# Performance work log

Hardware: AMD Instinct MI355X
Metric: run time of the kernel (lower is better)

## Reference

```python
import jax, jax.numpy as jnp
import numpy as np

N, IN_FEATS, OUT_FEATS = 8192, 512, 256


def setup_inputs() -> dict:
    key = jax.random.key(0)
    k1, k2, k3, k4 = jax.random.split(key, 4)
    feature_mat = jax.random.normal(k1, (N, IN_FEATS), dtype=jnp.float32)
    # Xavier-uniform style init for W and W2
    limW = float(np.sqrt(6.0 / (IN_FEATS + OUT_FEATS)))
    W = jax.random.uniform(k2, (IN_FEATS, OUT_FEATS), minval=-limW, maxval=limW, dtype=jnp.float32)
    limW2 = float(np.sqrt(6.0 / (2 * OUT_FEATS + 1)))
    W2 = jax.random.uniform(k3, (2 * OUT_FEATS, 1), minval=-limW2, maxval=limW2, dtype=jnp.float32)
    adj_mat = jax.random.randint(k4, (N, N), 0, 2, dtype=jnp.int32)
    return {"feature_mat": feature_mat, "W": W, "W2": W2, "adj_mat": adj_mat}


def reference(feature_mat, W, W2, adj_mat):
    out_feats = W.shape[1]
    Wh = feature_mat @ W                      # [N, F']
    Wh1 = Wh @ W2[:out_feats, :]              # [N, 1]
    Wh2 = Wh @ W2[out_feats:, :]              # [N, 1]
    e = Wh1 + Wh2.T                           # [N, N] broadcast add
    e = jnp.where(e > 0, e, 0.2 * e)          # leaky_relu(0.2)
    # NOTE: original masks with ZERO (not -inf) before softmax — faithful.
    e = jnp.where(adj_mat > 0, e, jnp.zeros((), dtype=e.dtype))
    attention = jax.nn.softmax(e, axis=1)     # row softmax over all N
    h_prime = attention @ Wh                  # [N, F']
    return jax.nn.relu(h_prime)
```

## Files before the change

### kernel.cpp

```cpp
#include <hip/hip_runtime.h>
#include <cstdint>
#include <cstddef>

#define NR 8192
#define FOUT 256
#define KIN 512
#define KSPLIT 4
#define JCHUNK (NR / KSPLIT)
#define BKJ 64
#define NSTEP (JCHUNK / BKJ)
#define IROWS 64

typedef __attribute__((ext_vector_type(8))) short bf16x8;
typedef __attribute__((ext_vector_type(4))) float f32x4;

__device__ __forceinline__ unsigned f2bf(float x) {
  unsigned u = __float_as_uint(x);
  u += 0x7fffu + ((u >> 16) & 1u);
  return u >> 16;
}
__device__ __forceinline__ float bf2f(unsigned h) {
  return __uint_as_float(h << 16);
}
__device__ __forceinline__ unsigned fkey(float x) {
  unsigned u = __float_as_uint(x);
  return (u & 0x80000000u) ? ~u : (u | 0x80000000u);
}
__device__ __forceinline__ float fkey_dec(unsigned k) {
  return __uint_as_float((k & 0x80000000u) ? (k ^ 0x80000000u) : ~k);
}

#define GLDS(g, l)                                                            \
  __builtin_amdgcn_global_load_lds(                                           \
      (const __attribute__((address_space(1))) unsigned int*)(g),             \
      (__attribute__((address_space(3))) unsigned int*)(l), 16, 0, 0)

__global__ __launch_bounds__(256) void k0_prep(const float* __restrict__ W,
                                               const float* __restrict__ W2,
                                               float* __restrict__ w1,
                                               float* __restrict__ w2,
                                               char* __restrict__ WTbf,
                                               unsigned* __restrict__ maxkey) {
  if (blockIdx.x == 0 && threadIdx.x == 0) *maxkey = 0u;
  int wv = threadIdx.x >> 6, lane = threadIdx.x & 63;
  int k = blockIdx.x * 4 + wv;
  int f4 = lane * 4;
  float4 wr = *(const float4*)(W + (size_t)k * FOUT + f4);
  float4 a = *(const float4*)(W2 + f4);
  float4 b = *(const float4*)(W2 + FOUT + f4);
  float d1 = wr.x * a.x + wr.y * a.y + wr.z * a.z + wr.w * a.w;
  float d2 = wr.x * b.x + wr.y * b.y + wr.z * b.z + wr.w * b.w;
#pragma unroll
  for (int off = 32; off; off >>= 1) {
    d1 += __shfl_xor(d1, off);
    d2 += __shfl_xor(d2, off);
  }
  if (lane == 0) {
    w1[k] = d1;
    w2[k] = d2;
  }
  int kt = k >> 5, kl = k & 31;
  float wv4[4] = {wr.x, wr.y, wr.z, wr.w};
#pragma unroll
  for (int ff = 0; ff < 4; ++ff) {
    int f = f4 + ff;
    size_t addr = (size_t)kt * 16384 + (f >> 4) * 1024 +
                  (((f & 15) | (((kl >> 3) & 3) << 4)) * 16) + (kl & 7) * 2;
    *(unsigned short*)(WTbf + addr) = (unsigned short)f2bf(wv4[ff]);
  }
}

__global__ __launch_bounds__(256) void k2_fused(
    const float* __restrict__ X, const char* __restrict__ WTbf,
    const float* __restrict__ w1, const float* __restrict__ w2,
    char* __restrict__ WhTf, float* __restrict__ Wh1, float* __restrict__ Wh2,
    unsigned* __restrict__ maxkey) {
  __shared__ char smem[2 * 18432 + 4096];
  char* buf0 = smem;
  char* buf1 = smem + 18432;
  char* wlds = smem + 2 * 18432;
  int t = threadIdx.x, wv = t >> 6, lane = t & 63;
  int jb = blockIdx.x * 32;
  int jr = t >> 3, koff = (t & 7) * 4;
  int cA = (jr & 15) | (((koff >> 3) & 3) << 4);
  int swA = cA ^ (((cA >> 4) & 3) << 2);
  int aoff = (jr >> 4) * 1024 + swA * 16 + ((koff & 4) << 1);
  int slotR = lane ^ (((lane >> 4) & 3) << 2);
  const float* xrow = X + (size_t)(jb + jr) * KIN + koff;

  {
    float2 a_ = *(const float2*)(w1 + t * 2);
    float2 b_ = *(const float2*)(w2 + t * 2);
    *(float2*)(wlds + t * 8) = a_;
    *(float2*)(wlds + 2048 + t * 8) = b_;
  }
  __syncthreads();

  float4 st0, st1, st2, st3;
  float d1 = 0.f, d2 = 0.f;
  f32x4 acc[2][4];
#pragma unroll
  for (int a = 0; a < 2; ++a)
#pragma unroll
    for (int b = 0; b < 4; ++b) acc[a][b] = (f32x4){0.f, 0.f, 0.f, 0.f};

#define K2_GLB(KT, BUFW)                                                      \
  do {                                                                        \
    const char* gs_ = WTbf + ((size_t)(KT) << 14) + (wv << 12) + lane * 16;   \
    char* ld_ = (BUFW) + 2048 + (wv << 12);                                   \
    GLDS(gs_, ld_);                                                           \
    GLDS(gs_ + 1024, ld_ + 1024);                                             \
    GLDS(gs_ + 2048, ld_ + 2048);                                             \
    GLDS(gs_ + 3072, ld_ + 3072);                                             \
  } while (0)

#define K2_LDX(KT, ST) (ST) = *(const float4*)(xrow + (KT) * 32)

#define K2_AGEN(ST, BUFW, SNUM)                                               \
  do {                                                                        \
    uint2 a_;                                                                 \
    a_.x = f2bf((ST).x) | (f2bf((ST).y) << 16);                               \
    a_.y = f2bf((ST).z) | (f2bf((ST).w) << 16);                               \
    *(uint2*)((BUFW) + aoff) = a_;                                            \
    float4 wa_ = *(const float4*)(wlds + ((SNUM)*32 + koff) * 4);             \
    float4 wb_ = *(const float4*)(wlds + 2048 + ((SNUM)*32 + koff) * 4);      \
    d1 += (ST).x * wa_.x + (ST).y * wa_.y + (ST).z * wa_.z + (ST).w * wa_.w;  \
    d2 += (ST).x * wb_.x + (ST).y * wb_.y + (ST).z * wb_.z + (ST).w * wb_.w;  \
  } while (0)

#define K2_ITER(S, BUFR, BUFW, STC, STF)                                      \
  do {                                                                        \
    int s_ = (S);                                                             \
    if (s_ + 1 < 16) K2_GLB(s_ + 1, BUFW);                                    \
    K2_LDX((s_ + 3 < 16) ? s_ + 3 : 15, STF);                                 \
    if (s_ + 1 < 16) K2_AGEN(STC, BUFW, s_ + 1);                              \
    bf16x8 a0 = *(const bf16x8*)((BUFR) + slotR * 16);                        \
    bf16x8 a1 = *(const bf16x8*)((BUFR) + 1024 + slotR * 16);                 \
    bf16x8 b0 = *(const bf16x8*)((BUFR) + 2048 + (wv * 4 + 0) * 1024 + lane * 16); \
    bf16x8 b1 = *(const bf16x8*)((BUFR) + 2048 + (wv * 4 + 1) * 1024 + lane * 16); \
    bf16x8 b2 = *(const bf16x8*)((BUFR) + 2048 + (wv * 4 + 2) * 1024 + lane * 16); \
    bf16x8 b3 = *(const bf16x8*)((BUFR) + 2048 + (wv * 4 + 3) * 1024 + lane * 16); \
    acc[0][0] = __builtin_amdgcn_mfma_f32_16x16x32_bf16(a0, b0, acc[0][0], 0, 0, 0); \
    acc[0][1] = __builtin_amdgcn_mfma_f32_16x16x32_bf16(a0, b1, acc[0][1], 0, 0, 0); \
    acc[0][2] = __builtin_amdgcn_mfma_f32_16x16x32_bf16(a0, b2, acc[0][2], 0, 0, 0); \
    acc[0][3] = __builtin_amdgcn_mfma_f32_16x16x32_bf16(a0, b3, acc[0][3], 0, 0, 0); \
    acc[1][0] = __builtin_amdgcn_mfma_f32_16x16x32_bf16(a1, b0, acc[1][0], 0, 0, 0); \
    acc[1][1] = __builtin_amdgcn_mfma_f32_16x16x32_bf16(a1, b1, acc[1][1], 0, 0, 0); \
    acc[1][2] = __builtin_amdgcn_mfma_f32_16x16x32_bf16(a1, b2, acc[1][2], 0, 0, 0); \
    acc[1][3] = __builtin_amdgcn_mfma_f32_16x16x32_bf16(a1, b3, acc[1][3], 0, 0, 0); \
    __builtin_amdgcn_sched_barrier(0);                                        \
    asm volatile("s_waitcnt vmcnt(1)");                                       \
    asm volatile("s_waitcnt lgkmcnt(0)");                                     \
    __builtin_amdgcn_s_barrier();                                             \
    __builtin_amdgcn_sched_barrier(0);                                        \
  } while (0)

  K2_GLB(0, buf0);
  K2_LDX(0, st0);
  K2_LDX(1, st1);
  K2_LDX(2, st2);
  K2_AGEN(st0, buf0, 0);
  __builtin_amdgcn_sched_barrier(0);
  asm volatile("s_waitcnt vmcnt(2)");
  asm volatile("s_waitcnt lgkmcnt(0)");
  __builtin_amdgcn_s_barrier();
  __builtin_amdgcn_sched_barrier(0);

  for (int s4 = 0; s4 < 16; s4 += 4) {
    K2_ITER(s4 + 0, buf0, buf1, st1, st3);
    K2_ITER(s4 + 1, buf1, buf0, st2, st0);
    K2_ITER(s4 + 2, buf0, buf1, st3, st1);
    K2_ITER(s4 + 3, buf1, buf0, st0, st2);
  }
#undef K2_ITER
#undef K2_AGEN
#undef K2_LDX
#undef K2_GLB

  int q = lane >> 4;
#pragma unroll
  for (int mi = 0; mi < 2; ++mi)
#pragma unroll
    for (int nn = 0; nn < 4; ++nn) {
      int u2 = wv * 4 + nn;
      int cell = (lane & 15) | ((((mi * 2) + (q >> 1)) & 3) << 4);
      uint2 v;
      v.x = f2bf(acc[mi][nn].x) | (f2bf(acc[mi][nn].y) << 16);
      v.y = f2bf(acc[mi][nn].z) | (f2bf(acc[mi][nn].w) << 16);
      *(uint2*)(buf0 + 2048 + u2 * 1024 + cell * 16 + ((q & 1) << 3)) = v;
    }
  __syncthreads();
  char* wb = WhTf + (size_t)blockIdx.x * 16384;
#pragma unroll
  for (int q2 = 0; q2 < 4; ++q2) {
    uint4 v = *(const uint4*)(buf0 + 2048 + q2 * 4096 + t * 16);
    *(uint4*)(wb + q2 * 4096 + t * 16) = v;
  }

  d1 += __shfl_xor(d1, 1);
  d1 += __shfl_xor(d1, 2);
  d1 += __shfl_xor(d1, 4);
  d2 += __shfl_xor(d2, 1);
  d2 += __shfl_xor(d2, 2);
  d2 += __shfl_xor(d2, 4);
  if ((t & 7) == 0) {
    Wh1[jb + jr] = d1;
    Wh2[jb + jr] = d2;
  }
  float mx = d2;
#pragma unroll
  for (int off = 32; off >= 8; off >>= 1) mx = fmaxf(mx, __shfl_xor(mx, off));
  __shared__ float red[4];
  if (lane == 0) red[wv] = mx;
  __syncthreads();
  if (t == 0) {
    float bm = fmaxf(fmaxf(red[0], red[1]), fmaxf(red[2], red[3]));
    atomicMax(maxkey, fkey(bm));
  }
}

__device__ __forceinline__ uint2 hv4(int4 aq, float4 wq, float wh1, float m,
                                     float enm, float& z) {
  float s0 = wh1 + wq.x, s1 = wh1 + wq.y, s2 = wh1 + wq.z, s3 = wh1 + wq.w;
  s0 = fmaxf(s0, 0.2f * s0);
  s1 = fmaxf(s1, 0.2f * s1);
  s2 = fmaxf(s2, 0.2f * s2);
  s3 = fmaxf(s3, 0.2f * s3);
  float w0 = aq.x > 0 ? __expf(s0 - m) : enm;
  float w1 = aq.y > 0 ? __expf(s1 - m) : enm;
  float w2 = aq.z > 0 ? __expf(s2 - m) : enm;
  float w3 = aq.w > 0 ? __expf(s3 - m) : enm;
  unsigned h0 = f2bf(w0), h1 = f2bf(w1), h2 = f2bf(w2), h3 = f2bf(w3);
  z += bf2f(h0) + bf2f(h1) + bf2f(h2) + bf2f(h3);
  uint2 r;
  r.x = h0 | (h1 << 16);
  r.y = h2 | (h3 << 16);
  return r;
}
__device__ __forceinline__ uint4 hv8(int4 a0, int4 a1, float4 w0, float4 w1,
                                     float wh1, float m, float enm, float& z) {
  uint2 r0 = hv4(a0, w0, wh1, m, enm, z);
  uint2 r1 = hv4(a1, w1, wh1, m, enm, z);
  return (uint4){r0.x, r0.y, r1.x, r1.y};
}

__global__ __launch_bounds__(512, 4) void k3_attn(
    const int* __restrict__ adj, const char* __restrict__ WhTf,
    const float* __restrict__ Wh1, const float* __restrict__ Wh2,
    const unsigned* __restrict__ maxptr, float* __restrict__ PVp,
    float* __restrict__ Zp) {
  __shared__ char smem[24576];
  char* abuf0 = smem;
  char* abuf1 = smem + 8192;
  char* wlds = smem + 16384;
  int t = threadIdx.x, wv = t >> 6, lane = t & 63;
  int kc = blockIdx.x & 3;
  int ib = blockIdx.x >> 2;
  int ibase = ib * IROWS;
  int jbch = kc * JCHUNK;
  int r0 = t >> 3;
  int j8 = (t & 7) * 8;
  int iglob = ibase + r0;
  float maxwh2 = fkey_dec(*maxptr);
  float wh1 = Wh1[iglob];
  float m = fmaxf(0.f, wh1 + maxwh2);
  float enm = __expf(-m);
  int unitA = (r0 >> 4) * 2 + (j8 >> 5);
  int cA = (r0 & 15) | (((j8 & 31) >> 3) << 4);
  int swA = cA ^ (((cA >> 4) & 3) << 2);
  int aoff = unitA * 1024 + swA * 16;
  int slotR = lane ^ (((lane >> 4) & 3) << 2);
  const int* adjrow = adj + ((size_t)iglob << 13) + jbch + j8;
  const char* bbase = WhTf + ((size_t)(kc * 64) << 14) + (size_t)(wv * 2) * 1024 +
                      (size_t)lane * 16;
  const char* wl = wlds + j8 * 4;

  *(float4*)(wlds + t * 16) = *(const float4*)(Wh2 + jbch + t * 4);
  __syncthreads();

  int4 st0_a, st0_b, st1_a, st1_b;
  f32x4 acc[4][2];
#pragma unroll
  for (int a = 0; a < 4; ++a)
#pragma unroll
    for (int b = 0; b < 2; ++b) acc[a][b] = (f32x4){0.f, 0.f, 0.f, 0.f};
  float zacc = 0.f;

#define K3_LDA(S, ST)                                                         \
  do {                                                                        \
    int sc_ = (S) < NSTEP ? (S) : NSTEP - 1;                                  \
    ST##_a = *(const int4*)(adjrow + sc_ * BKJ);                              \
    ST##_b = *(const int4*)(adjrow + sc_ * BKJ + 4);                          \
  } while (0)

#define K3_ITER(S, AR, AW, STC, DO_HV)                                        \
  do {                                                                        \
    int s_ = (S);                                                             \
    const char* bp_ = bbase + (size_t)(2 * s_) * 16384;                       \
    bf16x8 b00 = *(const bf16x8*)(bp_);                                       \
    bf16x8 b10 = *(const bf16x8*)(bp_ + 1024);                                \
    bf16x8 b01 = *(const bf16x8*)(bp_ + 16384);                               \
    bf16x8 b11 = *(const bf16x8*)(bp_ + 16384 + 1024);                        \
    if (DO_HV) {                                                              \
      float4 wq0_ = *(const float4*)(wl + (s_ + 1) * 256);                    \
      float4 wq1_ = *(const float4*)(wl + (s_ + 1) * 256 + 16);               \
      uint4 a_ = hv8(STC##_a, STC##_b, wq0_, wq1_, wh1, m, enm, zacc);        \
      *(uint4*)((AW) + aoff) = a_;                                            \
    }                                                                         \
    K3_LDA(s_ + 3, STC);                                                      \
    _Pragma("unroll")                                                         \
    for (int rf_ = 0; rf_ < 4; ++rf_) {                                       \
      bf16x8 ak0_ = *(const bf16x8*)((AR) + (rf_ * 2 + 0) * 1024 + slotR * 16); \
      bf16x8 ak1_ = *(const bf16x8*)((AR) + (rf_ * 2 + 1) * 1024 + slotR * 16); \
      acc[rf_][0] = __builtin_amdgcn_mfma_f32_16x16x32_bf16(ak0_, b00, acc[rf_][0], 0, 0, 0); \
      acc[rf_][1] = __builtin_amdgcn_mfma_f32_16x16x32_bf16(ak0_, b10, acc[rf_][1], 0, 0, 0); \
      acc[rf_][0] = __builtin_amdgcn_mfma_f32_16x16x32_bf16(ak1_, b01, acc[rf_][0], 0, 0, 0); \
      acc[rf_][1] = __builtin_amdgcn_mfma_f32_16x16x32_bf16(ak1_, b11, acc[rf_][1], 0, 0, 0); \
    }                                                                         \
    __builtin_amdgcn_sched_barrier(0);                                        \
    asm volatile("s_waitcnt lgkmcnt(0)" ::: "memory");                        \
    __builtin_amdgcn_s_barrier();                                             \
    __builtin_amdgcn_sched_barrier(0);                                        \
  } while (0)

  int4 adj0a = *(const int4*)(adjrow);
  int4 adj0b = *(const int4*)(adjrow + 4);
  K3_LDA(1, st1);
  K3_LDA(2, st0);
  {
    float4 wq0 = *(const float4*)(wl);
    float4 wq1 = *(const float4*)(wl + 16);
    uint4 a0 = hv8(adj0a, adj0b, wq0, wq1, wh1, m, enm, zacc);
    *(uint4*)(abuf0 + aoff) = a0;
  }
  __builtin_amdgcn_sched_barrier(0);
  asm volatile("s_waitcnt lgkmcnt(0)" ::: "memory");
  __builtin_amdgcn_s_barrier();
  __builtin_amdgcn_sched_barrier(0);

  for (int s2 = 0; s2 < NSTEP - 2; s2 += 2) {
    K3_ITER(s2 + 0, abuf0, abuf1, st1, 1);
    K3_ITER(s2 + 1, abuf1, abuf0, st0, 1);
  }
  K3_ITER(NSTEP - 2, abuf0, abuf1, st1, 1);
  K3_ITER(NSTEP - 1, abuf1, abuf0, st0, 0);
#undef K3_ITER
#undef K3_LDA

  zacc += __shfl_xor(zacc, 1);
  zacc += __shfl_xor(zacc, 2);
  zacc += __shfl_xor(zacc, 4);
  if ((t & 7) == 0) Zp[(size_t)kc * NR + iglob] = zacc;
#pragma unroll
  for (int rf = 0; rf < 4; ++rf)
#pragma unroll
    for (int un = 0; un < 2; ++un) {
      int f = (wv * 2 + un) * 16 + (lane & 15);
      int row0 = ibase + rf * 16 + ((lane >> 4) << 2);
      size_t base = ((size_t)kc * NR + row0) * FOUT + f;
      PVp[base + 0 * FOUT] = acc[rf][un].x;
      PVp[base + 1 * FOUT] = acc[rf][un].y;
      PVp[base + 2 * FOUT] = acc[rf][un].z;
      PVp[base + 3 * FOUT] = acc[rf][un].w;
    }
}

__global__ __launch_bounds__(256) void k4_reduce(const float* __restrict__ PVp,
                                                 const float* __restrict__ Zp,
                                                 float* __restrict__ out) {
  int tid = blockIdx.x * 256 + threadIdx.x;
  int i = tid >> 6;
  int f4 = (tid & 63) * 4;
  float z = Zp[i] + Zp[NR + i] + Zp[2 * NR + i] + Zp[3 * NR + i];
  float4 a = {0.f, 0.f, 0.f, 0.f};
#pragma unroll
  for (int c = 0; c < KSPLIT; ++c) {
    float4 p = *(const float4*)(PVp + ((size_t)c * NR + i) * FOUT + f4);
    a.x += p.x;
    a.y += p.y;
    a.z += p.z;
    a.w += p.w;
  }
  float inv = 1.f / z;
  float4 r;
  r.x = fmaxf(a.x * inv, 0.f);
  r.y = fmaxf(a.y * inv, 0.f);
  r.z = fmaxf(a.z * inv, 0.f);
  r.w = fmaxf(a.w * inv, 0.f);
  *(float4*)(out + (size_t)i * FOUT + f4) = r;
}

extern "C" void kernel_launch(void* const* d_in, const int* in_sizes, int n_in,
                              void* d_out, int out_size, void* d_ws,
                              size_t ws_size, hipStream_t stream) {
  const float* X = (const float*)d_in[0];
  const float* W = (const float*)d_in[1];
  const float* W2 = (const float*)d_in[2];
  const int* adj = (const int*)d_in[3];
  float* out = (float*)d_out;
  char* ws = (char*)d_ws;

  const size_t WHT_OFF = 0;
  const size_t WTBF_OFF = (size_t)4 * 1024 * 1024;
  const size_t W1_OFF = WTBF_OFF + 256 * 1024;
  const size_t W2V_OFF = W1_OFF + 2048;
  const size_t WH1_OFF = W2V_OFF + 2048;
  const size_t WH2_OFF = WH1_OFF + 32768;
  const size_t MXK_OFF = WH2_OFF + 32768;
  const size_t ZP_OFF = MXK_OFF + 256;
  const size_t PV_OFF = ZP_OFF + (size_t)KSPLIT * NR * 4;

  char* WhTf = ws + WHT_OFF;
  char* WTbf = ws + WTBF_OFF;
  float* w1 = (float*)(ws + W1_OFF);
  float* w2 = (float*)(ws + W2V_OFF);
  float* Wh1 = (float*)(ws + WH1_OFF);
  float* Wh2 = (float*)(ws + WH2_OFF);
  unsigned* maxkey = (unsigned*)(ws + MXK_OFF);
  float* Zp = (float*)(ws + ZP_OFF);
  float* PVp = (float*)(ws + PV_OFF);

  k0_prep<<<128, 256, 0, stream>>>(W, W2, w1, w2, WTbf, maxkey);
  k2_fused<<<256, 256, 0, stream>>>(X, WTbf, w1, w2, WhTf, Wh1, Wh2, maxkey);
  k3_attn<<<512, 512, 0, stream>>>(adj, WhTf, Wh1, Wh2, maxkey, PVp, Zp);
  k4_reduce<<<2048, 256, 0, stream>>>(PVp, Zp, out);
}
```

Before: 117.9 us.

## Double row tile per attention block and prefetch Wh B-operand one step ahead

The attention kernel now handles 128 rows per block with 1024 threads. Pairs of waves share the same feature columns and split the rows, so each global Wh fragment load feeds twice as many rows. The B-operand loads are also double-buffered in registers and issued one step ahead of the MFMAs to hide global latency. In exchange the grid is halved to 256 blocks, so fewer blocks are resident per CU. The larger block also raises LDS use and register pressure under the 1024-thread launch bound.

```diff
diff --git a/kernel.cpp b/kernel.cpp
--- a/kernel.cpp
+++ b/kernel.cpp
@@ -9,7 +9,7 @@
 #define JCHUNK (NR / KSPLIT)
 #define BKJ 64
 #define NSTEP (JCHUNK / BKJ)
-#define IROWS 64
+#define IROWS 128
 
 typedef __attribute__((ext_vector_type(8))) short bf16x8;
 typedef __attribute__((ext_vector_type(4))) float f32x4;
@@ -244,15 +244,15 @@
   return (uint4){r0.x, r0.y, r1.x, r1.y};
 }
 
-__global__ __launch_bounds__(512, 4) void k3_attn(
+__global__ __launch_bounds__(1024, 4) void k3_attn(
     const int* __restrict__ adj, const char* __restrict__ WhTf,
     const float* __restrict__ Wh1, const float* __restrict__ Wh2,
     const unsigned* __restrict__ maxptr, float* __restrict__ PVp,
     float* __restrict__ Zp) {
-  __shared__ char smem[24576];
+  __shared__ char smem[40960];
   char* abuf0 = smem;
-  char* abuf1 = smem + 8192;
-  char* wlds = smem + 16384;
+  char* abuf1 = smem + 16384;
+  char* wlds = smem + 32768;
   int t = threadIdx.x, wv = t >> 6, lane = t & 63;
   int kc = blockIdx.x & 3;
   int ib = blockIdx.x >> 2;
@@ -271,13 +271,15 @@
   int aoff = unitA * 1024 + swA * 16;
   int slotR = lane ^ (((lane >> 4) & 3) << 2);
   const int* adjrow = adj + ((size_t)iglob << 13) + jbch + j8;
-  const char* bbase = WhTf + ((size_t)(kc * 64) << 14) + (size_t)(wv * 2) * 1024 +
+  int g = wv >> 1, h = wv & 1;
+  const char* bbase = WhTf + ((size_t)(kc * 64) << 14) + (size_t)(2 * g) * 1024 +
                       (size_t)lane * 16;
   const char* wl = wlds + j8 * 4;
 
-  *(float4*)(wlds + t * 16) = *(const float4*)(Wh2 + jbch + t * 4);
+  *(float2*)(wlds + t * 8) = *(const float2*)(Wh2 + jbch + t * 2);
   __syncthreads();
 
+  bf16x8 bA00, bA01, bA10, bA11, bB00, bB01, bB10, bB11;
   int4 st0_a, st0_b, st1_a, st1_b;
   f32x4 acc[4][2];
 #pragma unroll
@@ -285,6 +287,16 @@
 #pragma unroll
     for (int b = 0; b < 2; ++b) acc[a][b] = (f32x4){0.f, 0.f, 0.f, 0.f};
   float zacc = 0.f;
+
+#define K3_LDB(S, B00, B01, B10, B11)                                         \
+  do {                                                                        \
+    int sc_ = (S) < NSTEP ? (S) : NSTEP - 1;                                  \
+    const char* bp_ = bbase + (size_t)(2 * sc_) * 16384;                      \
+    B00 = *(const bf16x8*)(bp_);                                 \
+    B01 = *(const bf16x8*)(bp_ + 16384);                         \
+    B10 = *(const bf16x8*)(bp_ + 1024);                          \
+    B11 = *(const bf16x8*)(bp_ + 16384 + 1024);                  \
+  } while (0)
 
 #define K3_LDA(S, ST)                                                         \
   do {                                                                        \
@@ -293,14 +305,11 @@
     ST##_b = *(const int4*)(adjrow + sc_ * BKJ + 4);                          \
   } while (0)
 
-#define K3_ITER(S, AR, AW, STC, DO_HV)                                        \
+#define K3_ITER(S, AR, AW, BC00, BC01, BC10, BC11, BF00, BF01, BF10, BF11,    \
+                STC, DO_HV)                                                   \
   do {                                                                        \
     int s_ = (S);                                                             \
-    const char* bp_ = bbase + (size_t)(2 * s_) * 16384;                       \
-    bf16x8 b00 = *(const bf16x8*)(bp_);                                       \
-    bf16x8 b10 = *(const bf16x8*)(bp_ + 1024);                                \
-    bf16x8 b01 = *(const bf16x8*)(bp_ + 16384);                               \
-    bf16x8 b11 = *(const bf16x8*)(bp_ + 16384 + 1024);                        \
+    K3_LDB(s_ + 1, BF00, BF01, BF10, BF11);                                   \
     if (DO_HV) {                                                              \
       float4 wq0_ = *(const float4*)(wl + (s_ + 1) * 256);                    \
       float4 wq1_ = *(const float4*)(wl + (s_ + 1) * 256 + 16);               \
@@ -310,12 +319,13 @@
     K3_LDA(s_ + 3, STC);                                                      \
     _Pragma("unroll")                                                         \
     for (int rf_ = 0; rf_ < 4; ++rf_) {                                       \
-      bf16x8 ak0_ = *(const bf16x8*)((AR) + (rf_ * 2 + 0) * 1024 + slotR * 16); \
-      bf16x8 ak1_ = *(const bf16x8*)((AR) + (rf_ * 2 + 1) * 1024 + slotR * 16); \
-      acc[rf_][0] = __builtin_amdgcn_mfma_f32_16x16x32_bf16(ak0_, b00, acc[rf_][0], 0, 0, 0); \
-      acc[rf_][1] = __builtin_amdgcn_mfma_f32_16x16x32_bf16(ak0_, b10, acc[rf_][1], 0, 0, 0); \
-      acc[rf_][0] = __builtin_amdgcn_mfma_f32_16x16x32_bf16(ak1_, b01, acc[rf_][0], 0, 0, 0); \
-      acc[rf_][1] = __builtin_amdgcn_mfma_f32_16x16x32_bf16(ak1_, b11, acc[rf_][1], 0, 0, 0); \
+      int ub_ = (h * 4 + rf_) * 2;                                            \
+      bf16x8 a0_ = *(const bf16x8*)((AR) + (ub_ + 0) * 1024 + slotR * 16);    \
+      bf16x8 a1_ = *(const bf16x8*)((AR) + (ub_ + 1) * 1024 + slotR * 16);    \
+      acc[rf_][0] = __builtin_amdgcn_mfma_f32_16x16x32_bf16(a0_, BC00, acc[rf_][0], 0, 0, 0); \
+      acc[rf_][1] = __builtin_amdgcn_mfma_f32_16x16x32_bf16(a0_, BC10, acc[rf_][1], 0, 0, 0); \
+      acc[rf_][0] = __builtin_amdgcn_mfma_f32_16x16x32_bf16(a1_, BC01, acc[rf_][0], 0, 0, 0); \
+      acc[rf_][1] = __builtin_amdgcn_mfma_f32_16x16x32_bf16(a1_, BC11, acc[rf_][1], 0, 0, 0); \
     }                                                                         \
     __builtin_amdgcn_sched_barrier(0);                                        \
     asm volatile("s_waitcnt lgkmcnt(0)" ::: "memory");                        \
@@ -323,6 +333,7 @@
     __builtin_amdgcn_sched_barrier(0);                                        \
   } while (0)
 
+  K3_LDB(0, bA00, bA01, bA10, bA11);
   int4 adj0a = *(const int4*)(adjrow);
   int4 adj0b = *(const int4*)(adjrow + 4);
   K3_LDA(1, st1);
@@ -339,13 +350,18 @@
   __builtin_amdgcn_sched_barrier(0);
 
   for (int s2 = 0; s2 < NSTEP - 2; s2 += 2) {
-    K3_ITER(s2 + 0, abuf0, abuf1, st1, 1);
-    K3_ITER(s2 + 1, abuf1, abuf0, st0, 1);
-  }
-  K3_ITER(NSTEP - 2, abuf0, abuf1, st1, 1);
-  K3_ITER(NSTEP - 1, abuf1, abuf0, st0, 0);
+    K3_ITER(s2 + 0, abuf0, abuf1, bA00, bA01, bA10, bA11, bB00, bB01, bB10,
+            bB11, st1, 1);
+    K3_ITER(s2 + 1, abuf1, abuf0, bB00, bB01, bB10, bB11, bA00, bA01, bA10,
+            bA11, st0, 1);
+  }
+  K3_ITER(NSTEP - 2, abuf0, abuf1, bA00, bA01, bA10, bA11, bB00, bB01, bB10,
+          bB11, st1, 1);
+  K3_ITER(NSTEP - 1, abuf1, abuf0, bB00, bB01, bB10, bB11, bA00, bA01, bA10,
+          bA11, st0, 0);
 #undef K3_ITER
 #undef K3_LDA
+#undef K3_LDB
 
   zacc += __shfl_xor(zacc, 1);
   zacc += __shfl_xor(zacc, 2);
@@ -355,8 +371,8 @@
   for (int rf = 0; rf < 4; ++rf)
 #pragma unroll
     for (int un = 0; un < 2; ++un) {
-      int f = (wv * 2 + un) * 16 + (lane & 15);
-      int row0 = ibase + rf * 16 + ((lane >> 4) << 2);
+      int f = (2 * g + un) * 16 + (lane & 15);
+      int row0 = ibase + (h * 4 + rf) * 16 + ((lane >> 4) << 2);
       size_t base = ((size_t)kc * NR + row0) * FOUT + f;
       PVp[base + 0 * FOUT] = acc[rf][un].x;
       PVp[base + 1 * FOUT] = acc[rf][un].y;
@@ -422,6 +438,6 @@
 
   k0_prep<<<128, 256, 0, stream>>>(W, W2, w1, w2, WTbf, maxkey);
   k2_fused<<<256, 256, 0, stream>>>(X, WTbf, w1, w2, WhTf, Wh1, Wh2, maxkey);
-  k3_attn<<<512, 512, 0, stream>>>(adj, WhTf, Wh1, Wh2, maxkey, PVp, Zp);
+  k3_attn<<<256, 1024, 0, stream>>>(adj, WhTf, Wh1, Wh2, maxkey, PVp, Zp);
   k4_reduce<<<2048, 256, 0, stream>>>(PVp, Zp, out);
 }
```

Result: no change. 115.8 us (-1.8%).
